# Kernel tuning notes

Hardware: AMD Instinct MI355X
Metric: run time of the kernel (lower is better)

The kernel has to match this reference:

```python
import jax, jax.numpy as jnp
import numpy as np

N, T, V, D = 32, 417, 25, 2
NODES = T * V            # 10425 nodes per sample graph
E = 80000                # static interframe edges, shared across batch
HID = 20                 # GCN hidden size
LH = 50                  # lstm hidden == d_model == fc_hidden
NH, FF, NL = 5, 2048, 3  # transformer heads / ffn dim / layers
CO = 85                  # conv1d out channels (in_channels == T)
NC = 6
NS = 2                   # n stacked (lstm, gcn) stages
SZ = int(T * 0.2)        # 83 sampled timesteps for loss1
EPS = 1e-5


def setup_inputs() -> dict:
    key = jax.random.key(0)
    ks = iter(jax.random.split(key, 80))
    def r(shape, s=0.1):
        return jax.random.normal(next(ks), shape, dtype=jnp.float32) * s
    inp = {
        "x": jax.random.normal(next(ks), (N, T, V * D), dtype=jnp.float32),
        "y": jax.random.randint(next(ks), (N,), 0, NC),
        "edge_index": jax.random.randint(next(ks), (2, E), 0, NODES),
        "idx2": jax.random.randint(next(ks), (N, SZ), 0, T - 1),
        "h0s": jax.random.normal(next(ks), (NS, N, LH), dtype=jnp.float32),
        "c0s": jax.random.normal(next(ks), (NS, N, LH), dtype=jnp.float32),
        # params; layouts are (in, out) so x @ W == torch x @ W.T
        "lstm_Wih": r((NS, LH, 4 * LH)),
        "lstm_Whh": r((NS, LH, 4 * LH)),
        "lstm_bih": r((NS, 4 * LH)),
        "lstm_bhh": r((NS, 4 * LH)),
        "gcn1_W": r((NS, D, HID)),
        "gcn1_b": r((NS, HID)),
        "bn_g": jnp.ones((NS, HID), jnp.float32),
        "bn_b": jnp.zeros((NS, HID), jnp.float32),
        "gcn2_W": r((NS, HID, D)),
        "gcn2_b": r((NS, D)),
        "fc_W": r((LH, LH)),
        "fc_b": r((LH,)),
        "conv_W": r((CO, T)),
        "conv_b": r((CO,)),
        "attn_inW": r((NL, LH, 3 * LH)),
        "attn_inb": r((NL, 3 * LH)),
        "attn_outW": r((NL, LH, LH)),
        "attn_outb": r((NL, LH)),
        "ff1W": r((NL, LH, FF)),
        "ff1b": r((NL, FF)),
        "ff2W": r((NL, FF, LH)),
        "ff2b": r((NL, LH)),
        "ln1g": jnp.ones((NL, LH), jnp.float32),
        "ln1b": jnp.zeros((NL, LH), jnp.float32),
        "ln2g": jnp.ones((NL, LH), jnp.float32),
        "ln2b": jnp.zeros((NL, LH), jnp.float32),
        "Wc1": r((CO * LH, LH), 0.02),
        "bc1": r((LH,)),
        "Wc2": r((LH, NC)),
        "bc2": r((NC,)),
    }
    return inp


def _lstm(x, Wih, Whh, bih, bhh, h0, c0):
    # x: (N,T,in); single layer, batch_first; gate order i,f,g,o (torch)
    def step(carry, xt):
        h, c = carry
        g = xt @ Wih + h @ Whh + bih + bhh
        i, f, gg, o = jnp.split(g, 4, axis=-1)
        c = jax.nn.sigmoid(f) * c + jax.nn.sigmoid(i) * jnp.tanh(gg)
        h = jax.nn.sigmoid(o) * jnp.tanh(c)
        return (h, c), h
    _, hs = jax.lax.scan(step, (h0, c0), jnp.swapaxes(x, 0, 1))
    return jnp.swapaxes(hs, 0, 1)


def _gcn(X, W, b, src, dst, norm):
    # PyG GCNConv: x @ W, symmetric-normalized mean over neighbors (+self loops), + bias
    H = X @ W                                   # (N, NODES, out)
    msg = H[:, src, :] * norm[None, :, None]    # (N, E+NODES, out)
    agg = jax.vmap(lambda m: jax.ops.segment_sum(m, dst, num_segments=NODES))(msg)
    return agg + b


def _ln(x, g, b):
    m = x.mean(-1, keepdims=True)
    v = ((x - m) ** 2).mean(-1, keepdims=True)
    return (x - m) * jax.lax.rsqrt(v + EPS) * g + b


def _mha(x, inW, inb, outW, outb):
    # torch batch_first=False semantics: x is (S, B, E); here S=N, B=CO
    S, B, Em = x.shape
    hd = Em // NH
    qkv = x @ inW + inb
    q, k, v = jnp.split(qkv, 3, axis=-1)
    q = q.reshape(S, B, NH, hd)
    k = k.reshape(S, B, NH, hd)
    v = v.reshape(S, B, NH, hd)
    att = jnp.einsum('sbhd,tbhd->bhst', q, k) * (jnp.float32(hd) ** -0.5)
    w = jax.nn.softmax(att, axis=-1)
    o = jnp.einsum('bhst,tbhd->sbhd', w, v).reshape(S, B, Em)
    return o @ outW + outb


def _forward(x, y, edge_index, idx2, h0s, c0s,
             lstm_Wih, lstm_Whh, lstm_bih, lstm_bhh,
             gcn1_W, gcn1_b, bn_g, bn_b, gcn2_W, gcn2_b,
             fc_W, fc_b, conv_W, conv_b,
             attn_inW, attn_inb, attn_outW, attn_outb,
             ff1W, ff1b, ff2W, ff2b, ln1g, ln1b, ln2g, ln2b,
             Wc1, bc1, Wc2, bc2):
    loops = jnp.arange(NODES)
    src = jnp.concatenate([edge_index[0], loops])
    dst = jnp.concatenate([edge_index[1], loops])
    deg = jax.ops.segment_sum(jnp.ones(src.shape[0], jnp.float32), dst, num_segments=NODES)
    dinv = jnp.where(deg > 0, deg ** -0.5, 0.0)
    norm = dinv[src] * dinv[dst]

    x1 = x
    for s in range(NS):
        x1 = _lstm(x1, lstm_Wih[s], lstm_Whh[s], lstm_bih[s], lstm_bhh[s], h0s[s], c0s[s])
        xg = x1.reshape(N, NODES, D)
        h = _gcn(xg, gcn1_W[s], gcn1_b[s], src, dst, norm)
        # BatchNorm1d over all nodes of the whole batched graph (training stats)
        hf = h.reshape(-1, HID)
        m = hf.mean(0)
        v = hf.var(0)
        h = (h - m) * jax.lax.rsqrt(v + EPS) * bn_g[s] + bn_b[s]
        h = jax.nn.relu(h)
        xg = _gcn(h, gcn2_W[s], gcn2_b[s], src, dst, norm)
        x1 = xg.reshape(N, T, V * D)

    # unsupervised next-frame loss (Dropout is eval-mode identity)
    x_b1 = x1 @ fc_W + fc_b
    rows = jnp.arange(N)[:, None]
    pred = x_b1[rows, idx2]
    tgt = x[rows, idx2 + 1]
    loss1 = jnp.mean((pred - tgt) ** 2)

    # Conv1d(417->85, k=1) over time-as-channels
    t = jnp.einsum('oc,ncl->nol', conv_W, x1) + conv_b[None, :, None]  # (N, CO, LH)
    # torch encoder treats dim0=N as sequence, dim1=CO as batch (post-norm layers)
    for l in range(NL):
        a = _mha(t, attn_inW[l], attn_inb[l], attn_outW[l], attn_outb[l])
        t = _ln(t + a, ln1g[l], ln1b[l])
        f = jax.nn.relu(t @ ff1W[l] + ff1b[l]) @ ff2W[l] + ff2b[l]
        t = _ln(t + f, ln2g[l], ln2b[l])

    flat = t.reshape(N, CO * LH)
    h1 = jax.nn.relu(flat @ Wc1 + bc1)
    logits = h1 @ Wc2 + bc2
    logp = jax.nn.log_softmax(logits, axis=-1)
    loss2 = -jnp.mean(logp[jnp.arange(N), y])
    return jnp.exp(logp), loss1, loss2


def reference(x, y, edge_index, idx2, h0s, c0s,
              lstm_Wih, lstm_Whh, lstm_bih, lstm_bhh,
              gcn1_W, gcn1_b, bn_g, bn_b, gcn2_W, gcn2_b,
              fc_W, fc_b, conv_W, conv_b,
              attn_inW, attn_inb, attn_outW, attn_outb,
              ff1W, ff1b, ff2W, ff2b, ln1g, ln1b, ln2g, ln2b,
              Wc1, bc1, Wc2, bc2):
    return _forward(x, y, edge_index, idx2, h0s, c0s,
                    lstm_Wih, lstm_Whh, lstm_bih, lstm_bhh,
                    gcn1_W, gcn1_b, bn_g, bn_b, gcn2_W, gcn2_b,
                    fc_W, fc_b, conv_W, conv_b,
                    attn_inW, attn_inb, attn_outW, attn_outb,
                    ff1W, ff1b, ff2W, ff2b, ln1g, ln1b, ln2g, ln2b,
                    Wc1, bc1, Wc2, bc2)
```

## Files before the change

kernel.cpp:

```cpp
#include <hip/hip_runtime.h>
#include <math.h>

#define N_ 32
#define T_ 417
#define V_ 25
#define D_ 2
#define NODES_ 10425
#define E_ 80000
#define EN_ (E_ + NODES_)
#define HID_ 20
#define LH_ 50
#define NH_ 5
#define HD_ 10
#define FF_ 2048
#define NL_ 3
#define CO_ 85
#define NC_ 6
#define NS_ 2
#define SZ_ 83
#define EPS_ 1e-5f
#define NCH_ 11
#define NBNB_ 1304

__device__ inline float sane(float v){
  return (v == v && fabsf(v) < 1e30f) ? v : 0.f;
}

__device__ inline float wave_sum(float v){
  #pragma unroll
  for (int off = 32; off > 0; off >>= 1) v += __shfl_xor(v, off, 64);
  return v;
}

__global__ void k_init(const float* __restrict__ x, float* __restrict__ x1,
                       int* __restrict__ deg, float* __restrict__ accs){
  int i = blockIdx.x * 256 + threadIdx.x;
  if (i < N_*T_*LH_) x1[i] = x[i];
  if (i < NODES_) deg[i] = 0;
  if (i < 8) accs[i] = 0.f;
}

__global__ void k_deg(const int* __restrict__ ei, int* __restrict__ deg){
  int e = blockIdx.x * 256 + threadIdx.x;
  if (e >= EN_) return;
  int d = (e < E_) ? ei[E_ + e] : (e - E_);
  if ((unsigned)d >= NODES_) d = 0;
  atomicAdd(&deg[d], 1);
}

__global__ __launch_bounds__(256) void k_chunksum(const int* __restrict__ deg, int* __restrict__ csum){
  __shared__ int red[256];
  int chunk = blockIdx.x, tid = threadIdx.x;
  int s = 0;
  for (int i = tid; i < 1024; i += 256){
    int g = chunk*1024 + i;
    s += (g < NODES_) ? deg[g] : 0;
  }
  red[tid] = s;
  __syncthreads();
  for (int off = 128; off > 0; off >>= 1){
    if (tid < off) red[tid] += red[tid + off];
    __syncthreads();
  }
  if (tid == 0) csum[chunk] = red[0];
}

__global__ void k_chunkscan(int* __restrict__ csum){
  if (threadIdx.x == 0 && blockIdx.x == 0){
    int run = 0;
    for (int i = 0; i < NCH_; i++){ int t = csum[i]; csum[i] = run; run += t; }
  }
}

__global__ __launch_bounds__(1024) void k_scan2(const int* __restrict__ deg, const int* __restrict__ csum,
                       int* __restrict__ rowoff, int* __restrict__ wp, float* __restrict__ dinv){
  __shared__ int sdata[1024];
  int chunk = blockIdx.x, tid = threadIdx.x;
  int g = chunk*1024 + tid;
  int v = (g < NODES_) ? deg[g] : 0;
  int xv = v;
  sdata[tid] = xv;
  __syncthreads();
  for (int off = 1; off < 1024; off <<= 1){
    int add = (tid >= off) ? sdata[tid - off] : 0;
    __syncthreads();
    xv += add;
    sdata[tid] = xv;
    __syncthreads();
  }
  if (g < NODES_){
    int excl = csum[chunk] + xv - v;
    rowoff[g] = excl;
    wp[g] = excl;
    dinv[g] = (v > 0) ? rsqrtf((float)v) : 0.f;
  }
}

__global__ void k_scatter(const int* __restrict__ ei, const float* __restrict__ dinv,
                          int* __restrict__ wp, int* __restrict__ col, float* __restrict__ val){
  int e = blockIdx.x * 256 + threadIdx.x;
  if (e >= EN_) return;
  int s, d;
  if (e < E_){ s = ei[e]; d = ei[E_ + e]; } else { s = d = e - E_; }
  if ((unsigned)s >= NODES_) s = 0;
  if ((unsigned)d >= NODES_) d = 0;
  int pos = atomicAdd(&wp[d], 1);
  if ((unsigned)pos < EN_){
    col[pos] = s;
    val[pos] = dinv[s] * dinv[d];
  }
}

__global__ void k_xw(const float* __restrict__ x1, const float* __restrict__ Wih,
                     const float* __restrict__ bih, const float* __restrict__ bhh,
                     float* __restrict__ xW, int s){
  int idx = blockIdx.x * 256 + threadIdx.x;
  if (idx >= N_*T_*200) return;
  int r = idx / 200, g = idx % 200;
  const float* W = Wih + s*LH_*200;
  const float* xr = x1 + r*LH_;
  float acc = bih[s*200+g] + bhh[s*200+g];
  #pragma unroll 10
  for (int k = 0; k < LH_; k++) acc += xr[k] * W[k*200 + g];
  xW[idx] = acc;
}

__global__ __launch_bounds__(256) void k_lstm(const float* __restrict__ xW, float* __restrict__ x1,
                       const float* __restrict__ Whh, const float* __restrict__ h0,
                       const float* __restrict__ c0, int s){
  __shared__ float hsw[4][52];
  __shared__ float gates[2][200];
  __shared__ float hist[64][LH_];
  int n = blockIdx.x, tid = threadIdx.x;
  int w = tid >> 6;
  int l = tid & 63;
  int gcol = (tid < 200) ? tid : 199;
  float wcol[LH_];
  {
    const float* W = Whh + s*LH_*200 + gcol;
    #pragma unroll
    for (int k = 0; k < LH_; k++) wcol[k] = W[k*200];
  }
  float c = 0.f;
  if (l < LH_){
    c = c0[s*N_*LH_ + n*LH_ + l];
    hsw[w][l] = h0[s*N_*LH_ + n*LH_ + l];
  }
  if (l >= LH_ && l < 52) hsw[w][l] = 0.f;
  __syncthreads();
  const float* xwn = xW + (size_t)n*T_*200;
  float* out = x1 + (size_t)n*T_*LH_;
  float xnext = (tid < 200) ? xwn[tid] : 0.f;
  for (int t = 0; t < T_; t++){
    float hreg[52];
    {
      const float4* hp = (const float4*)&hsw[w][0];
      #pragma unroll
      for (int k4 = 0; k4 < 13; k4++){
        float4 hv = hp[k4];
        hreg[k4*4]   = hv.x;
        hreg[k4*4+1] = hv.y;
        hreg[k4*4+2] = hv.z;
        hreg[k4*4+3] = hv.w;
      }
    }
    float acc = xnext;
    if (t + 1 < T_) xnext = (tid < 200) ? xwn[(t+1)*200 + tid] : 0.f;
    #pragma unroll
    for (int k = 0; k < LH_; k++) acc += hreg[k] * wcol[k];
    if (tid < 200) gates[t & 1][tid] = acc;
    __syncthreads();
    if (l < LH_){
      const float* gb = gates[t & 1];
      float gi = gb[l], gf = gb[LH_+l], gg = gb[100+l], go = gb[150+l];
      float si = 1.f/(1.f + __expf(-gi));
      float sf = 1.f/(1.f + __expf(-gf));
      float so = 1.f/(1.f + __expf(-go));
      float tg = tanhf(gg);
      c = sf*c + si*tg;
      float h = so * tanhf(c);
      hsw[w][l] = h;
      if (w == 0) hist[t & 63][l] = h;
    }
    if ((t & 63) == 63 || t == T_ - 1){
      __syncthreads();
      int cnt = ((t & 63) + 1) * LH_;
      int tbase = t - (t & 63);
      const float* hf = &hist[0][0];
      for (int idx = tid; idx < cnt; idx += 256)
        out[tbase*LH_ + idx] = hf[idx];
      __syncthreads();
    }
  }
}

__global__ void k_tonode(const float* __restrict__ x1, float* __restrict__ P0){
  int idx = blockIdx.x * 256 + threadIdx.x;
  if (idx >= NODES_*64) return;
  int v = idx >> 6, rem = idx & 63;
  int n = rem >> 1, d = rem & 1;
  P0[idx] = x1[n*(T_*LH_) + v*D_ + d];
}

__global__ __launch_bounds__(64) void k_gather(const int* __restrict__ rowoff, const int* __restrict__ deg,
                       const int* __restrict__ col, const float* __restrict__ val,
                       const float* __restrict__ src, float* __restrict__ dst){
  int v = blockIdx.x, tid = threadIdx.x;
  int start = rowoff[v], len = deg[v];
  float acc = 0.f;
  for (int j = 0; j < len; j++){
    int cs = col[start + j];
    if ((unsigned)cs >= NODES_) cs = 0;
    acc += val[start + j] * src[cs*64 + tid];
  }
  dst[v*64 + tid] = acc;
}

__global__ __launch_bounds__(256) void k_bnstat(const float* __restrict__ P1, float* __restrict__ bnpart){
  int idx = blockIdx.x * 256 + threadIdx.x;
  float p0 = 0.f, p1v = 0.f;
  if (idx < NODES_*N_){ p0 = P1[idx*2]; p1v = P1[idx*2+1]; }
  float sv[5] = {p0, p1v, p0*p0, p1v*p1v, p0*p1v};
  __shared__ float red[5][4];
  int wave = threadIdx.x >> 6, lane = threadIdx.x & 63;
  #pragma unroll
  for (int j = 0; j < 5; j++){
    float w = wave_sum(sv[j]);
    if (lane == 0) red[j][wave] = w;
  }
  __syncthreads();
  if (threadIdx.x < 5){
    int j = threadIdx.x;
    bnpart[j*NBNB_ + blockIdx.x] = red[j][0] + red[j][1] + red[j][2] + red[j][3];
  }
}

__global__ __launch_bounds__(256) void k_bnfin(const float* __restrict__ bnpart,
                        const float* __restrict__ W1, const float* __restrict__ b1,
                        const float* __restrict__ bn_g, const float* __restrict__ bn_b,
                        float* __restrict__ bnsc, int s){
  __shared__ float red[256];
  __shared__ float S[5];
  int tid = threadIdx.x;
  for (int j = 0; j < 5; j++){
    float acc = 0.f;
    for (int t = tid; t < NBNB_; t += 256) acc += bnpart[j*NBNB_ + t];
    red[tid] = acc;
    __syncthreads();
    for (int off = 128; off > 0; off >>= 1){
      if (tid < off) red[tid] += red[tid + off];
      __syncthreads();
    }
    if (tid == 0) S[j] = red[0];
    __syncthreads();
  }
  if (tid < HID_){
    int c = tid;
    const float M = (float)(N_*NODES_);
    float w0 = W1[s*D_*HID_ + c], w1 = W1[s*D_*HID_ + HID_ + c];
    float bc = b1[s*HID_ + c];
    float m0 = S[0]/M, m1 = S[1]/M;
    float e00 = S[2]/M, e11 = S[3]/M, e01 = S[4]/M;
    float mean = w0*m0 + w1*m1 + bc;
    float v00 = e00 - m0*m0, v11 = e11 - m1*m1, c01 = e01 - m0*m1;
    float var = w0*w0*v00 + w1*w1*v11 + 2.f*w0*w1*c01;
    var = fmaxf(var, 0.f);
    float sc = bn_g[s*HID_ + c] * rsqrtf(var + EPS_);
    bnsc[c] = sc;
    bnsc[HID_ + c] = bn_b[s*HID_ + c] - mean*sc;
  }
}

__global__ __launch_bounds__(256) void k_bnrelu_t2(const float* __restrict__ P1, const float* __restrict__ bnsc,
                            const float* __restrict__ W1, const float* __restrict__ b1,
                            const float* __restrict__ W2, float* __restrict__ Rb, int s){
  int idx = blockIdx.x * 256 + threadIdx.x;
  if (idx >= NODES_*N_) return;
  float p0 = P1[idx*2], p1v = P1[idx*2+1];
  const float* W1p = W1 + s*D_*HID_;
  const float* W2p = W2 + s*HID_*D_;
  float a0 = 0.f, a1 = 0.f;
  #pragma unroll
  for (int c = 0; c < HID_; c++){
    float q = p0*W1p[c] + p1v*W1p[HID_ + c] + b1[s*HID_ + c];
    float h = fmaxf(q*bnsc[c] + bnsc[HID_ + c], 0.f);
    a0 += h * W2p[c*D_];
    a1 += h * W2p[c*D_ + 1];
  }
  Rb[idx*2]     = a0;
  Rb[idx*2 + 1] = a1;
}

__global__ __launch_bounds__(64) void k_gcn2(const int* __restrict__ rowoff, const int* __restrict__ deg,
                      const int* __restrict__ col, const float* __restrict__ val,
                      const float* __restrict__ Rb, const float* __restrict__ gb2,
                      float* __restrict__ x1, int s){
  int v = blockIdx.x, tid = threadIdx.x;
  int start = rowoff[v], len = deg[v];
  float acc = 0.f;
  for (int j = 0; j < len; j++){
    int cs = col[start + j];
    if ((unsigned)cs >= NODES_) cs = 0;
    acc += val[start + j] * Rb[cs*64 + tid];
  }
  int n = tid >> 1, d = tid & 1;
  x1[n*(T_*LH_) + v*D_ + d] = acc + gb2[s*D_ + d];
}

__global__ __launch_bounds__(64) void k_loss1(const float* __restrict__ x1, const float* __restrict__ x,
                       const int* __restrict__ idx2, const float* __restrict__ fcW,
                       const float* __restrict__ fcb, float* __restrict__ accs){
  int bi = blockIdx.x;
  int n = bi / SZ_, j = bi % SZ_;
  int row = idx2[n*SZ_ + j];
  if ((unsigned)row >= (T_ - 1)) row = 0;
  int l = threadIdx.x;
  float sq = 0.f;
  if (l < LH_){
    const float* xr = x1 + n*T_*LH_ + row*LH_;
    float acc = fcb[l];
    #pragma unroll 10
    for (int k = 0; k < LH_; k++) acc += xr[k] * fcW[k*LH_ + l];
    float dd = acc - x[n*T_*LH_ + (row+1)*LH_ + l];
    sq = dd*dd;
  }
  sq = wave_sum(sq);
  if (l == 0) atomicAdd(&accs[0], sq);
}

__global__ __launch_bounds__(64) void k_conv(const float* __restrict__ x1, const float* __restrict__ cW,
                      const float* __restrict__ cb, float* __restrict__ tb){
  int bi = blockIdx.x;
  int n = bi / CO_, o = bi % CO_;
  int l = threadIdx.x;
  if (l >= LH_) return;
  float acc = cb[o];
  const float* w = cW + o*T_;
  const float* xr = x1 + n*T_*LH_ + l;
  #pragma unroll 4
  for (int c2 = 0; c2 < T_; c2++) acc += w[c2] * xr[c2*LH_];
  tb[bi*LH_ + l] = acc;
}

__global__ void k_qkv(const float* __restrict__ tb, const float* __restrict__ inW,
                      const float* __restrict__ inb, float* __restrict__ qkv, int l3){
  int idx = blockIdx.x * 256 + threadIdx.x;
  if (idx >= N_*CO_*150) return;
  int r = idx / 150, j = idx % 150;
  const float* W = inW + l3*LH_*150;
  const float* tr = tb + r*LH_;
  float acc = inb[l3*150 + j];
  #pragma unroll 10
  for (int k = 0; k < LH_; k++) acc += tr[k] * W[k*150 + j];
  qkv[idx] = acc;
}

__global__ __launch_bounds__(128) void k_attn(const float* __restrict__ qkv, float* __restrict__ abuf){
  __shared__ float qs[32][HD_], ks[32][HD_], vs[32][HD_], att[32][32];
  int bi = blockIdx.x;
  int b = bi % CO_, h = bi / CO_;
  int tid = threadIdx.x;
  for (int idx = tid; idx < 960; idx += 128){
    int grp = idx / 320, m = idx % 320, ss = m / HD_, dd = m % HD_;
    float vvv = qkv[(ss*CO_ + b)*150 + grp*LH_ + h*HD_ + dd];
    if (grp == 0) qs[ss][dd] = vvv;
    else if (grp == 1) ks[ss][dd] = vvv;
    else vs[ss][dd] = vvv;
  }
  __syncthreads();
  const float scale = 0.31622776601683794f;
  for (int idx = tid; idx < 1024; idx += 128){
    int ss = idx >> 5, tt = idx & 31;
    float a = 0.f;
    #pragma unroll
    for (int dd = 0; dd < HD_; dd++) a += qs[ss][dd]*ks[tt][dd];
    att[ss][tt] = a*scale;
  }
  __syncthreads();
  if (tid < 32){
    float m = -1e31f;
    for (int tt = 0; tt < 32; tt++) m = fmaxf(m, att[tid][tt]);
    float sum = 0.f;
    for (int tt = 0; tt < 32; tt++){ float e = __expf(att[tid][tt] - m); att[tid][tt] = e; sum += e; }
    float inv = 1.f / fmaxf(sum, 1e-30f);
    for (int tt = 0; tt < 32; tt++) att[tid][tt] *= inv;
  }
  __syncthreads();
  for (int idx = tid; idx < 320; idx += 128){
    int ss = idx / HD_, dd = idx % HD_;
    float acc = 0.f;
    #pragma unroll
    for (int tt = 0; tt < 32; tt++) acc += att[ss][tt]*vs[tt][dd];
    abuf[(ss*CO_ + b)*LH_ + h*HD_ + dd] = acc;
  }
}

__global__ __launch_bounds__(64) void k_proj_ln(float* __restrict__ tb, const float* __restrict__ abuf,
                         const float* __restrict__ outW, const float* __restrict__ outb,
                         const float* __restrict__ g, const float* __restrict__ bb, int l3){
  __shared__ float orow[LH_];
  int r = blockIdx.x, l = threadIdx.x;
  if (l < LH_) orow[l] = abuf[r*LH_ + l];
  __syncthreads();
  float rr = 0.f;
  if (l < LH_){
    const float* W = outW + l3*LH_*LH_;
    float p = outb[l3*LH_ + l];
    #pragma unroll 10
    for (int k = 0; k < LH_; k++) p += orow[k] * W[k*LH_ + l];
    rr = tb[r*LH_ + l] + p;
  }
  float mean = wave_sum(rr) / (float)LH_;
  float dv = (l < LH_) ? (rr - mean) : 0.f;
  float var = wave_sum(dv*dv) / (float)LH_;
  if (l < LH_)
    tb[r*LH_ + l] = (rr - mean)*rsqrtf(var + EPS_)*g[l3*LH_ + l] + bb[l3*LH_ + l];
}

__global__ __launch_bounds__(512) void k_ff(float* __restrict__ tb, const float* __restrict__ w1,
                     const float* __restrict__ bi1, const float* __restrict__ w2,
                     const float* __restrict__ bi2, const float* __restrict__ g,
                     const float* __restrict__ bb, int l3){
  __shared__ float tin[2][LH_];
  __shared__ float hb0[FF_], hb1[FF_];
  __shared__ float part[2][8][LH_];
  int r0 = blockIdx.x * 2, tid = threadIdx.x;
  if (tid < 2*LH_) tin[tid/LH_][tid%LH_] = tb[r0*LH_ + tid];
  __syncthreads();
  const float* W1l = w1 + l3*LH_*FF_;
  #pragma unroll
  for (int i = 0; i < 4; i++){
    int j = i*512 + tid;
    float bj = bi1[l3*FF_ + j];
    float a0 = bj, a1 = bj;
    #pragma unroll 10
    for (int k = 0; k < LH_; k++){
      float w = W1l[k*FF_ + j];
      a0 += tin[0][k]*w;
      a1 += tin[1][k]*w;
    }
    hb0[j] = fmaxf(a0, 0.f);
    hb1[j] = fmaxf(a1, 0.f);
  }
  __syncthreads();
  const float* W2l = w2 + l3*FF_*LH_;
  int l = tid & 63, grp = tid >> 6;
  if (l < LH_){
    float a0 = 0.f, a1 = 0.f;
    int jbase = grp * 256;
    const float* wp = W2l + (size_t)jbase*LH_ + l;
    #pragma unroll 4
    for (int jj = 0; jj < 256; jj++){
      float w = wp[jj*LH_];
      a0 += hb0[jbase + jj]*w;
      a1 += hb1[jbase + jj]*w;
    }
    part[0][grp][l] = a0;
    part[1][grp][l] = a1;
  }
  __syncthreads();
  if (tid < 128){
    int row = tid >> 6, ll = tid & 63;
    float out = 0.f;
    if (ll < LH_){
      float a = 0.f;
      #pragma unroll
      for (int gg = 0; gg < 8; gg++) a += part[row][gg][ll];
      out = a + bi2[l3*LH_ + ll] + tin[row][ll];
    }
    float s1 = (ll < LH_) ? out : 0.f;
    float mean = wave_sum(s1) / (float)LH_;
    float dv = (ll < LH_) ? (out - mean) : 0.f;
    float var = wave_sum(dv*dv) / (float)LH_;
    if (ll < LH_)
      tb[(r0 + row)*LH_ + ll] = (out - mean)*rsqrtf(var + EPS_)*g[l3*LH_ + ll] + bb[l3*LH_ + ll];
  }
}

__global__ __launch_bounds__(512) void k_head(const float* __restrict__ tb, const int* __restrict__ y,
                       const float* __restrict__ Wc1, const float* __restrict__ bc1,
                       const float* __restrict__ Wc2, const float* __restrict__ bc2,
                       float* __restrict__ out, float* __restrict__ accs){
  __shared__ float part[8][LH_];
  __shared__ float h1[LH_];
  __shared__ float lgs[NC_];
  int n = blockIdx.x, tid = threadIdx.x;
  int l = tid & 63, grp = tid >> 6;
  const float* tr = tb + n*CO_*LH_;
  if (l < LH_){
    int k0 = grp * 532;
    int k1 = k0 + 532; if (k1 > CO_*LH_) k1 = CO_*LH_;
    float acc = 0.f;
    for (int k = k0; k < k1; k++) acc += tr[k] * Wc1[k*LH_ + l];
    part[grp][l] = acc;
  }
  __syncthreads();
  if (tid < LH_){
    float a = bc1[tid];
    #pragma unroll
    for (int gg = 0; gg < 8; gg++) a += part[gg][tid];
    h1[tid] = fmaxf(a, 0.f);
  }
  __syncthreads();
  if (tid < NC_){
    float a = bc2[tid];
    #pragma unroll 10
    for (int k = 0; k < LH_; k++) a += h1[k] * Wc2[k*NC_ + tid];
    lgs[tid] = a;
  }
  __syncthreads();
  if (tid == 0){
    float m = -1e31f;
    for (int c2 = 0; c2 < NC_; c2++) m = fmaxf(m, lgs[c2]);
    float sum = 0.f;
    for (int c2 = 0; c2 < NC_; c2++) sum += __expf(lgs[c2] - m);
    float lse = m + logf(fmaxf(sum, 1e-30f));
    for (int c2 = 0; c2 < NC_; c2++)
      out[n*NC_ + c2] = __expf(lgs[c2] - lse);
    int yy = y[n];
    if ((unsigned)yy >= NC_) yy = 0;
    atomicAdd(&accs[1], -(lgs[yy] - lse));
  }
}

__global__ void k_fin(const float* __restrict__ accs, float* __restrict__ out){
  if (threadIdx.x == 0 && blockIdx.x == 0){
    out[N_*NC_]     = sane(accs[0] / (float)(N_*SZ_*LH_));
    out[N_*NC_ + 1] = sane(accs[1] / (float)N_);
  }
}

extern "C" void kernel_launch(void* const* d_in, const int* in_sizes, int n_in,
                              void* d_out, int out_size, void* d_ws, size_t ws_size,
                              hipStream_t stream){
  static const int expect[36] = {
    667200, 32, 160000, 2656, 3200, 3200,
    20000, 20000, 400, 400,
    80, 40, 40, 40, 80, 4,
    2500, 50, 35445, 85,
    22500, 450, 7500, 150,
    307200, 6144, 307200, 150,
    150, 150, 150, 150,
    212500, 50, 300, 6
  };
  if (n_in != 36 || out_size != 194 || ws_size < 14300000) return;
  for (int i = 0; i < 36; i++) if (in_sizes[i] != expect[i]) return;

  const float* x        = (const float*)d_in[0];
  const int*   y        = (const int*)d_in[1];
  const int*   ei       = (const int*)d_in[2];
  const int*   idx2     = (const int*)d_in[3];
  const float* h0s      = (const float*)d_in[4];
  const float* c0s      = (const float*)d_in[5];
  const float* lstm_Wih = (const float*)d_in[6];
  const float* lstm_Whh = (const float*)d_in[7];
  const float* lstm_bih = (const float*)d_in[8];
  const float* lstm_bhh = (const float*)d_in[9];
  const float* gcn1_W   = (const float*)d_in[10];
  const float* gcn1_b   = (const float*)d_in[11];
  const float* bn_g     = (const float*)d_in[12];
  const float* bn_b     = (const float*)d_in[13];
  const float* gcn2_W   = (const float*)d_in[14];
  const float* gcn2_b   = (const float*)d_in[15];
  const float* fc_W     = (const float*)d_in[16];
  const float* fc_b     = (const float*)d_in[17];
  const float* conv_W   = (const float*)d_in[18];
  const float* conv_b   = (const float*)d_in[19];
  const float* attn_inW = (const float*)d_in[20];
  const float* attn_inb = (const float*)d_in[21];
  const float* attn_outW= (const float*)d_in[22];
  const float* attn_outb= (const float*)d_in[23];
  const float* ff1W     = (const float*)d_in[24];
  const float* ff1b     = (const float*)d_in[25];
  const float* ff2W     = (const float*)d_in[26];
  const float* ff2b     = (const float*)d_in[27];
  const float* ln1g     = (const float*)d_in[28];
  const float* ln1b     = (const float*)d_in[29];
  const float* ln2g     = (const float*)d_in[30];
  const float* ln2b     = (const float*)d_in[31];
  const float* Wc1      = (const float*)d_in[32];
  const float* bc1      = (const float*)d_in[33];
  const float* Wc2      = (const float*)d_in[34];
  const float* bc2      = (const float*)d_in[35];
  float* out = (float*)d_out;

  char* wsp = (char*)d_ws;
  size_t off = 0;
  auto alloc = [&](size_t bytes)->void*{
    void* p = wsp + off;
    off = (off + bytes + 255) & ~(size_t)255;
    return p;
  };
  float* x1   = (float*)alloc((size_t)N_*T_*LH_*4);
  float* X    = (float*)alloc((size_t)N_*T_*200*4);
  float* val  = (float*)alloc((size_t)EN_*4);
  float* dinv = (float*)alloc((size_t)NODES_*4);
  float* bnsc = (float*)alloc(64*4);
  float* accs = (float*)alloc(8*4);
  int*   deg  = (int*)alloc((size_t)NODES_*4);
  int*   rowoff = (int*)alloc((size_t)(NODES_+1)*4);
  int*   wp   = (int*)alloc((size_t)NODES_*4);
  int*   col  = (int*)alloc((size_t)EN_*4);
  int*   csum = (int*)alloc(16*4);
  float* xW     = X;
  float* P0     = X;
  float* P1     = X + (size_t)NODES_*64;
  float* bnpart = X + (size_t)2*NODES_*64;
  float* Rb     = P0;
  float* tb     = X;
  float* qkvb   = X + 136064;
  float* abuf   = X + 544128;

  k_init<<<dim3((N_*T_*LH_ + 255)/256), dim3(256), 0, stream>>>(x, x1, deg, accs);
  k_deg<<<dim3((EN_ + 255)/256), dim3(256), 0, stream>>>(ei, deg);
  k_chunksum<<<dim3(NCH_), dim3(256), 0, stream>>>(deg, csum);
  k_chunkscan<<<dim3(1), dim3(64), 0, stream>>>(csum);
  k_scan2<<<dim3(NCH_), dim3(1024), 0, stream>>>(deg, csum, rowoff, wp, dinv);
  k_scatter<<<dim3((EN_ + 255)/256), dim3(256), 0, stream>>>(ei, dinv, wp, col, val);

  for (int s = 0; s < NS_; s++){
    k_xw<<<dim3((N_*T_*200 + 255)/256), dim3(256), 0, stream>>>(x1, lstm_Wih, lstm_bih, lstm_bhh, xW, s);
    k_lstm<<<dim3(N_), dim3(256), 0, stream>>>(xW, x1, lstm_Whh, h0s, c0s, s);
    k_tonode<<<dim3((NODES_*64 + 255)/256), dim3(256), 0, stream>>>(x1, P0);
    k_gather<<<dim3(NODES_), dim3(64), 0, stream>>>(rowoff, deg, col, val, P0, P1);
    k_bnstat<<<dim3(NBNB_), dim3(256), 0, stream>>>(P1, bnpart);
    k_bnfin<<<dim3(1), dim3(256), 0, stream>>>(bnpart, gcn1_W, gcn1_b, bn_g, bn_b, bnsc, s);
    k_bnrelu_t2<<<dim3((N_*NODES_ + 255)/256), dim3(256), 0, stream>>>(P1, bnsc, gcn1_W, gcn1_b, gcn2_W, Rb, s);
    k_gcn2<<<dim3(NODES_), dim3(64), 0, stream>>>(rowoff, deg, col, val, Rb, gcn2_b, x1, s);
  }

  k_loss1<<<dim3(N_*SZ_), dim3(64), 0, stream>>>(x1, x, idx2, fc_W, fc_b, accs);
  k_conv<<<dim3(N_*CO_), dim3(64), 0, stream>>>(x1, conv_W, conv_b, tb);

  for (int l3 = 0; l3 < NL_; l3++){
    k_qkv<<<dim3((N_*CO_*150 + 255)/256), dim3(256), 0, stream>>>(tb, attn_inW, attn_inb, qkvb, l3);
    k_attn<<<dim3(NH_*CO_), dim3(128), 0, stream>>>(qkvb, abuf);
    k_proj_ln<<<dim3(N_*CO_), dim3(64), 0, stream>>>(tb, abuf, attn_outW, attn_outb, ln1g, ln1b, l3);
    k_ff<<<dim3(N_*CO_/2), dim3(512), 0, stream>>>(tb, ff1W, ff1b, ff2W, ff2b, ln2g, ln2b, l3);
  }

  k_head<<<dim3(N_), dim3(512), 0, stream>>>(tb, y, Wc1, bc1, Wc2, bc2, out, accs);
  k_fin<<<dim3(1), dim3(64), 0, stream>>>(accs, out);
}
```

Baseline: 1.388 ms.

## Stage LSTM input projections in shared memory per chunk and speed gate math

```diff
diff --git a/kernel.cpp b/kernel.cpp
--- a/kernel.cpp
+++ b/kernel.cpp
@@ -21,6 +21,7 @@
 #define EPS_ 1e-5f
 #define NCH_ 11
 #define NBNB_ 1304
+#define LCH_ 32
 
 __device__ inline float sane(float v){
   return (v == v && fabsf(v) < 1e30f) ? v : 0.f;
@@ -130,7 +131,8 @@
                        const float* __restrict__ c0, int s){
   __shared__ float hsw[4][52];
   __shared__ float gates[2][200];
-  __shared__ float hist[64][LH_];
+  __shared__ float xs[LCH_*200];
+  __shared__ float hist[LCH_*LH_];
   int n = blockIdx.x, tid = threadIdx.x;
   int w = tid >> 6;
   int l = tid & 63;
@@ -147,50 +149,58 @@
     hsw[w][l] = h0[s*N_*LH_ + n*LH_ + l];
   }
   if (l >= LH_ && l < 52) hsw[w][l] = 0.f;
-  __syncthreads();
   const float* xwn = xW + (size_t)n*T_*200;
   float* out = x1 + (size_t)n*T_*LH_;
-  float xnext = (tid < 200) ? xwn[tid] : 0.f;
-  for (int t = 0; t < T_; t++){
-    float hreg[52];
-    {
-      const float4* hp = (const float4*)&hsw[w][0];
+  for (int t0 = 0; t0 < T_; t0 += LCH_){
+    int nst = T_ - t0; if (nst > LCH_) nst = LCH_;
+    int cnt = nst*200;
+    for (int idx = tid; idx < cnt; idx += 256) xs[idx] = xwn[t0*200 + idx];
+    __syncthreads();
+    for (int i = 0; i < nst; i++){
+      int t = t0 + i;
+      float hreg[52];
+      {
+        const float4* hp = (const float4*)&hsw[w][0];
+        #pragma unroll
+        for (int k4 = 0; k4 < 13; k4++){
+          float4 hv = hp[k4];
+          hreg[k4*4]   = hv.x;
+          hreg[k4*4+1] = hv.y;
+          hreg[k4*4+2] = hv.z;
+          hreg[k4*4+3] = hv.w;
+        }
+      }
+      float a0 = 0.f, a1 = 0.f, a2 = 0.f, a3 = 0.f;
       #pragma unroll
-      for (int k4 = 0; k4 < 13; k4++){
-        float4 hv = hp[k4];
-        hreg[k4*4]   = hv.x;
-        hreg[k4*4+1] = hv.y;
-        hreg[k4*4+2] = hv.z;
-        hreg[k4*4+3] = hv.w;
+      for (int k = 0; k < 48; k += 4){
+        a0 += hreg[k]  *wcol[k];
+        a1 += hreg[k+1]*wcol[k+1];
+        a2 += hreg[k+2]*wcol[k+2];
+        a3 += hreg[k+3]*wcol[k+3];
+      }
+      a0 += hreg[48]*wcol[48];
+      a1 += hreg[49]*wcol[49];
+      float acc = xs[i*200 + gcol] + ((a0 + a1) + (a2 + a3));
+      if (tid < 200) gates[t & 1][tid] = acc;
+      __syncthreads();
+      if (l < LH_){
+        const float* gb = gates[t & 1];
+        float gi = gb[l], gf = gb[LH_+l], gg = gb[100+l], go = gb[150+l];
+        float si = __frcp_rn(1.f + __expf(-gi));
+        float sf = __frcp_rn(1.f + __expf(-gf));
+        float so = __frcp_rn(1.f + __expf(-go));
+        float eg = __expf(2.f*gg);
+        float tg = 1.f - 2.f*__frcp_rn(eg + 1.f);
+        c = sf*c + si*tg;
+        float ec = __expf(2.f*c);
+        float h = so * (1.f - 2.f*__frcp_rn(ec + 1.f));
+        hsw[w][l] = h;
+        if (w == 0) hist[i*LH_ + l] = h;
       }
     }
-    float acc = xnext;
-    if (t + 1 < T_) xnext = (tid < 200) ? xwn[(t+1)*200 + tid] : 0.f;
-    #pragma unroll
-    for (int k = 0; k < LH_; k++) acc += hreg[k] * wcol[k];
-    if (tid < 200) gates[t & 1][tid] = acc;
     __syncthreads();
-    if (l < LH_){
-      const float* gb = gates[t & 1];
-      float gi = gb[l], gf = gb[LH_+l], gg = gb[100+l], go = gb[150+l];
-      float si = 1.f/(1.f + __expf(-gi));
-      float sf = 1.f/(1.f + __expf(-gf));
-      float so = 1.f/(1.f + __expf(-go));
-      float tg = tanhf(gg);
-      c = sf*c + si*tg;
-      float h = so * tanhf(c);
-      hsw[w][l] = h;
-      if (w == 0) hist[t & 63][l] = h;
-    }
-    if ((t & 63) == 63 || t == T_ - 1){
-      __syncthreads();
-      int cnt = ((t & 63) + 1) * LH_;
-      int tbase = t - (t & 63);
-      const float* hf = &hist[0][0];
-      for (int idx = tid; idx < cnt; idx += 256)
-        out[tbase*LH_ + idx] = hf[idx];
-      __syncthreads();
-    }
+    int hcnt = nst*LH_;
+    for (int idx = tid; idx < hcnt; idx += 256) out[t0*LH_ + idx] = hist[idx];
   }
 }
 
```

New measurement: 1.383 ms. Within noise of the previous version (-0.3%).
